# Performance work log

Measured on AMD Instinct MI355X. Metric: run time of the kernel, lower is better.

## Reference

```python
import math
import jax, jax.numpy as jnp
import numpy as np

NUM_HEADS = 16


def apply_rope(q, k, position_ids, dim):
    # q, k: [N, S, H, Dh]; position_ids: [S]
    half = dim // 2
    j = jnp.arange(half, dtype=q.dtype)
    theta = 1.0 / (10000.0 ** (2.0 * j / dim))                 # [half]
    angles = position_ids.astype(jnp.float32)[:, None] * theta[None, :]  # [S, half]
    cos = jnp.cos(angles)[None, :, None, :]                    # [1, S, 1, half]
    sin = jnp.sin(angles)[None, :, None, :]
    q1, q2 = q[..., :half], q[..., half:]
    k1, k2 = k[..., :half], k[..., half:]
    q_rot = jnp.concatenate([q1 * cos - q2 * sin, q1 * sin + q2 * cos], axis=-1)
    k_rot = jnp.concatenate([k1 * cos - k2 * sin, k1 * sin + k2 * cos], axis=-1)
    return q_rot, k_rot


def setup_inputs() -> dict:
    key = jax.random.key(0)
    ks = jax.random.split(key, 6)
    N, S, H = 2, 2048, 2048
    scale = 1.0 / math.sqrt(H)  # ~xavier magnitude
    X = jax.random.normal(ks[0], (N, S, H), dtype=jnp.float32)
    Wq = jax.random.normal(ks[1], (H, H), dtype=jnp.float32) * scale
    Wk = jax.random.normal(ks[2], (H, H), dtype=jnp.float32) * scale
    Wv = jax.random.normal(ks[3], (H, H), dtype=jnp.float32) * scale
    Wo = jax.random.normal(ks[4], (H, H), dtype=jnp.float32) * scale
    bo = jnp.zeros((H,), dtype=jnp.float32)
    position_ids = jnp.arange(S, dtype=jnp.int64 if jax.config.jax_enable_x64 else jnp.int32)
    mask = jnp.tril(jnp.ones((S, S), dtype=jnp.int32))  # causal
    return {"X": X, "position_ids": position_ids, "mask": mask,
            "Wq": Wq, "Wk": Wk, "Wv": Wv, "Wo": Wo, "bo": bo}


def reference(X, position_ids, mask, Wq, Wk, Wv, Wo, bo):
    N, S, H = X.shape
    nh = NUM_HEADS
    dh = H // nh
    # projections -> [N, S, nh, dh]
    Q = (X @ Wq.T).reshape(N, S, nh, dh)
    K = (X @ Wk.T).reshape(N, S, nh, dh)
    V = (X @ Wv.T).reshape(N, S, nh, dh)
    Q, K = apply_rope(Q, K, position_ids, dh)
    scores = jnp.einsum('bqhd,bkhd->bhqk', Q, K) / math.sqrt(dh)  # [N, nh, S, S]
    scores = jnp.where(mask[None, None, :, :] == 0, -jnp.inf, scores)
    weights = jax.nn.softmax(scores, axis=-1)
    context = jnp.einsum('bhqk,bkhd->bqhd', weights, V).reshape(N, S, H)
    return context @ Wo.T + bo
```

## Files before the change

### kernel.cpp

```cpp
#include <hip/hip_runtime.h>
#include <hip/hip_bf16.h>
#include <stdint.h>

typedef unsigned short u16;
typedef __attribute__((ext_vector_type(4))) float f32x4;
typedef __attribute__((ext_vector_type(8))) short s16x8;
typedef __attribute__((ext_vector_type(8))) __bf16 b16x8;

constexpr int NB = 2, SEQ = 2048, HD = 2048, NHEADS = 16, DHEAD = 128;
constexpr int MROWS = NB * SEQ;

__device__ __forceinline__ u16 f2b(float f) {
  __hip_bfloat16 h = __float2bfloat16(f);
  return __builtin_bit_cast(u16, h);
}
__device__ __forceinline__ float b2f(u16 u) {
  return __bfloat162float(__builtin_bit_cast(__hip_bfloat16, u));
}
__device__ __forceinline__ f32x4 mfma_bf16(s16x8 a, s16x8 b, f32x4 c) {
  return __builtin_amdgcn_mfma_f32_16x16x32_bf16(
      __builtin_bit_cast(b16x8, a), __builtin_bit_cast(b16x8, b), c, 0, 0, 0);
}
__device__ __forceinline__ void gload_lds16(const void* g, void* l) {
  __builtin_amdgcn_global_load_lds(
      (__attribute__((address_space(1))) void*)(const_cast<void*>(g)),
      (__attribute__((address_space(3))) void*)(l), 16, 0, 0);
}

__global__ void cvt_bf16(const float* __restrict__ in, u16* __restrict__ out, int n8) {
  int i = blockIdx.x * blockDim.x + threadIdx.x;
  if (i >= n8) return;
  const float4* p = (const float4*)(in + (size_t)i * 8);
  float4 a = p[0], b = p[1];
  ushort4* q = (ushort4*)(out + (size_t)i * 8);
  q[0] = make_ushort4(f2b(a.x), f2b(a.y), f2b(a.z), f2b(a.w));
  q[1] = make_ushort4(f2b(b.x), f2b(b.y), f2b(b.z), f2b(b.w));
}

template <bool FBIAS>
__global__ __launch_bounds__(256, 2) void gemm_nt(
    const u16* __restrict__ A, const u16* __restrict__ B, void* __restrict__ Cv,
    const float* __restrict__ bias, int Kd, int Nd) {
  __shared__ __align__(16) u16 Alds[128 * 32];
  __shared__ __align__(16) u16 Blds[128 * 32];
  const int t = threadIdx.x;
  const int lane = t & 63, w = t >> 6;
  const int lr = lane & 15, lg = lane >> 4;
  const int wr = (w >> 1) * 64, wc = (w & 1) * 64;
  const int trow = blockIdx.y * 128, tcol = blockIdx.x * 128;

  f32x4 acc[4][4] = {};

  const int c0 = t, c1 = t + 256;
  const u16* gA0 = A + (size_t)(trow + (c0 >> 2)) * Kd + (c0 & 3) * 8;
  const u16* gA1 = A + (size_t)(trow + (c1 >> 2)) * Kd + (c1 & 3) * 8;
  const u16* gB0 = B + (size_t)(tcol + (c0 >> 2)) * Kd + (c0 & 3) * 8;
  const u16* gB1 = B + (size_t)(tcol + (c1 >> 2)) * Kd + (c1 & 3) * 8;
  u16* lA0 = Alds + c0 * 8; u16* lA1 = Alds + c1 * 8;
  u16* lB0 = Blds + c0 * 8; u16* lB1 = Blds + c1 * 8;

  for (int kk = 0; kk < Kd; kk += 32) {
    gload_lds16(gA0 + kk, lA0);
    gload_lds16(gA1 + kk, lA1);
    gload_lds16(gB0 + kk, lB0);
    gload_lds16(gB1 + kk, lB1);
    __syncthreads();
    s16x8 af[4], bf[4];
#pragma unroll
    for (int m = 0; m < 4; ++m)
      af[m] = *(const s16x8*)(Alds + (wr + m * 16 + lr) * 32 + lg * 8);
#pragma unroll
    for (int nn = 0; nn < 4; ++nn)
      bf[nn] = *(const s16x8*)(Blds + (wc + nn * 16 + lr) * 32 + lg * 8);
#pragma unroll
    for (int m = 0; m < 4; ++m)
#pragma unroll
      for (int nn = 0; nn < 4; ++nn)
        acc[m][nn] = mfma_bf16(af[m], bf[nn], acc[m][nn]);
    __syncthreads();
  }

#pragma unroll
  for (int m = 0; m < 4; ++m)
#pragma unroll
    for (int nn = 0; nn < 4; ++nn)
#pragma unroll
      for (int r = 0; r < 4; ++r) {
        int row = trow + wr + m * 16 + lg * 4 + r;
        int col = tcol + wc + nn * 16 + lr;
        if constexpr (FBIAS)
          ((float*)Cv)[(size_t)row * Nd + col] = acc[m][nn][r] + bias[col];
        else
          ((u16*)Cv)[(size_t)row * Nd + col] = f2b(acc[m][nn][r]);
      }
}

__global__ void rope_inplace(u16* __restrict__ Qb, u16* __restrict__ Kb,
                             const int* __restrict__ pos) {
  int idx = blockIdx.x * blockDim.x + threadIdx.x;
  int row = idx >> 10;
  int pr = idx & 1023;
  int h = pr >> 6, j = pr & 63;
  int s = row & (SEQ - 1);
  float theta = expf(-0.14391156831f * (float)j);
  float ang = (float)pos[s] * theta;
  float sn, cs;
  sincosf(ang, &sn, &cs);
  size_t base = (size_t)row * HD + h * 128 + j;
  float q1 = b2f(Qb[base]), q2 = b2f(Qb[base + 64]);
  Qb[base] = f2b(q1 * cs - q2 * sn);
  Qb[base + 64] = f2b(q1 * sn + q2 * cs);
  float k1 = b2f(Kb[base]), k2 = b2f(Kb[base + 64]);
  Kb[base] = f2b(k1 * cs - k2 * sn);
  Kb[base + 64] = f2b(k1 * sn + k2 * cs);
}

__global__ __launch_bounds__(256, 4) void attn_fwd(
    const u16* __restrict__ Qb, const u16* __restrict__ Kb,
    const u16* __restrict__ Vt, u16* __restrict__ Ctx) {
  __shared__ __align__(16) u16 Klds[64 * 128];
  __shared__ __align__(16) u16 Vlds[128 * 64];
  __shared__ __align__(16) u16 Plds[4][16 * 64];

  const int t = threadIdx.x;
  const int lane = t & 63, w = t >> 6;
  const int lr = lane & 15, lg = lane >> 4;
  const int qt = (int)gridDim.x - 1 - (int)blockIdx.x;
  const int h = blockIdx.y, n = blockIdx.z;
  const int q0 = qt * 64 + w * 16;
  const size_t hoff = (size_t)h * DHEAD;

  s16x8 qf[4];
#pragma unroll
  for (int c = 0; c < 4; ++c)
    qf[c] = *(const s16x8*)(Qb + (size_t)(n * SEQ + q0 + lr) * HD + hoff + c * 32 + lg * 8);

  f32x4 o[8] = {};
  float mrow[4] = {-1e30f, -1e30f, -1e30f, -1e30f};
  float lsum[4] = {0.f, 0.f, 0.f, 0.f};

  const int nkt = qt + 1;

  for (int kt = 0; kt < nkt; ++kt) {
#pragma unroll
    for (int p = 0; p < 4; ++p) {
      int q = p * 256 + t;
      int r = q >> 4, cs = (q & 15) ^ (r & 7);
      gload_lds16(Kb + (size_t)(n * SEQ + kt * 64 + r) * HD + hoff + cs * 8,
                  Klds + q * 8);
    }
#pragma unroll
    for (int p = 0; p < 4; ++p) {
      int q = p * 256 + t;
      int r = q >> 3, cs = (q & 7) ^ (r & 7);
      gload_lds16(Vt + (size_t)(hoff + r) * MROWS + n * SEQ + kt * 64 + cs * 8,
                  Vlds + q * 8);
    }
    __syncthreads();

    f32x4 sc[4];
#pragma unroll
    for (int kb = 0; kb < 4; ++kb) {
      f32x4 a = {0.f, 0.f, 0.f, 0.f};
#pragma unroll
      for (int c = 0; c < 4; ++c) {
        s16x8 kf = *(const s16x8*)(Klds + (kb * 16 + lr) * 128 +
                                   (((c * 4 + lg) ^ (lr & 7))) * 8);
        a = mfma_bf16(qf[c], kf, a);
      }
      sc[kb] = a;
    }

    constexpr float scale = 0.08838834764831845f;
    float tmax[4] = {-1e30f, -1e30f, -1e30f, -1e30f};
#pragma unroll
    for (int r = 0; r < 4; ++r) {
      int qg = q0 + lg * 4 + r;
#pragma unroll
      for (int kb = 0; kb < 4; ++kb) {
        float s = sc[kb][r] * scale;
        if (kt * 64 + kb * 16 + lr > qg) s = -1e30f;
        sc[kb][r] = s;
        tmax[r] = fmaxf(tmax[r], s);
      }
    }
#pragma unroll
    for (int off = 1; off < 16; off <<= 1)
#pragma unroll
      for (int r = 0; r < 4; ++r)
        tmax[r] = fmaxf(tmax[r], __shfl_xor(tmax[r], off));

    float corr[4], rsum[4];
#pragma unroll
    for (int r = 0; r < 4; ++r) {
      float mnew = fmaxf(mrow[r], tmax[r]);
      corr[r] = __expf(mrow[r] - mnew);
      mrow[r] = mnew;
      rsum[r] = 0.f;
      int prow = lg * 4 + r;
#pragma unroll
      for (int kb = 0; kb < 4; ++kb) {
        float pv = __expf(sc[kb][r] - mnew);
        rsum[r] += pv;
        int col = kb * 16 + lr;
        Plds[w][prow * 64 + ((col >> 3) ^ (prow & 7)) * 8 + (col & 7)] = f2b(pv);
      }
    }
#pragma unroll
    for (int off = 1; off < 16; off <<= 1)
#pragma unroll
      for (int r = 0; r < 4; ++r) rsum[r] += __shfl_xor(rsum[r], off);
#pragma unroll
    for (int r = 0; r < 4; ++r) lsum[r] = lsum[r] * corr[r] + rsum[r];
#pragma unroll
    for (int nb = 0; nb < 8; ++nb)
#pragma unroll
      for (int r = 0; r < 4; ++r) o[nb][r] *= corr[r];

    s16x8 pf0 = *(const s16x8*)(&Plds[w][lr * 64 + ((lg) ^ (lr & 7)) * 8]);
    s16x8 pf1 = *(const s16x8*)(&Plds[w][lr * 64 + ((4 + lg) ^ (lr & 7)) * 8]);
#pragma unroll
    for (int nb = 0; nb < 8; ++nb) {
      int vrow = nb * 16 + lr;
      s16x8 vf0 = *(const s16x8*)(Vlds + vrow * 64 + ((lg) ^ (lr & 7)) * 8);
      s16x8 vf1 = *(const s16x8*)(Vlds + vrow * 64 + ((4 + lg) ^ (lr & 7)) * 8);
      o[nb] = mfma_bf16(pf0, vf0, o[nb]);
      o[nb] = mfma_bf16(pf1, vf1, o[nb]);
    }
    __syncthreads();
  }

  float inv[4];
#pragma unroll
  for (int r = 0; r < 4; ++r) inv[r] = 1.0f / lsum[r];
#pragma unroll
  for (int nb = 0; nb < 8; ++nb)
#pragma unroll
    for (int r = 0; r < 4; ++r)
      Ctx[(size_t)(n * SEQ + q0 + lg * 4 + r) * HD + hoff + nb * 16 + lr] =
          f2b(o[nb][r] * inv[r]);
}

extern "C" void kernel_launch(void* const* d_in, const int* in_sizes, int n_in,
                              void* d_out, int out_size, void* d_ws, size_t ws_size,
                              hipStream_t stream) {
  (void)in_sizes; (void)n_in; (void)out_size; (void)ws_size;
  const float* X  = (const float*)d_in[0];
  const int*  pos = (const int*)d_in[1];
  const float* Wq = (const float*)d_in[3];
  const float* Wk = (const float*)d_in[4];
  const float* Wv = (const float*)d_in[5];
  const float* Wo = (const float*)d_in[6];
  const float* bo = (const float*)d_in[7];
  float* out = (float*)d_out;

  constexpr size_t XE = (size_t)MROWS * HD;
  constexpr size_t WE = (size_t)HD * HD;

  char* p = (char*)d_ws;
  u16* Xb  = (u16*)p; p += XE * 2;
  u16* Wqb = (u16*)p; p += WE * 2;
  u16* Wkb = (u16*)p; p += WE * 2;
  u16* Wvb = (u16*)p; p += WE * 2;
  u16* Wob = (u16*)p; p += WE * 2;
  u16* Qb  = (u16*)p; p += XE * 2;
  u16* Kb  = (u16*)p; p += XE * 2;
  u16* Vtb = (u16*)p; p += XE * 2;
  u16* Ctx = Xb;

  cvt_bf16<<<(int)(XE / 8 / 256), 256, 0, stream>>>(X, Xb, (int)(XE / 8));
  cvt_bf16<<<(int)(WE / 8 / 256), 256, 0, stream>>>(Wq, Wqb, (int)(WE / 8));
  cvt_bf16<<<(int)(WE / 8 / 256), 256, 0, stream>>>(Wk, Wkb, (int)(WE / 8));
  cvt_bf16<<<(int)(WE / 8 / 256), 256, 0, stream>>>(Wv, Wvb, (int)(WE / 8));
  cvt_bf16<<<(int)(WE / 8 / 256), 256, 0, stream>>>(Wo, Wob, (int)(WE / 8));

  dim3 g(HD / 128, MROWS / 128);
  gemm_nt<false><<<g, 256, 0, stream>>>(Xb, Wqb, Qb, nullptr, HD, HD);
  gemm_nt<false><<<g, 256, 0, stream>>>(Xb, Wkb, Kb, nullptr, HD, HD);
  dim3 gv(MROWS / 128, HD / 128);
  gemm_nt<false><<<gv, 256, 0, stream>>>(Wvb, Xb, Vtb, nullptr, HD, MROWS);

  rope_inplace<<<MROWS * 1024 / 256, 256, 0, stream>>>(Qb, Kb, pos);

  attn_fwd<<<dim3(SEQ / 64, NHEADS, NB), 256, 0, stream>>>(Qb, Kb, Vtb, Ctx);

  gemm_nt<true><<<g, 256, 0, stream>>>(Ctx, Wob, out, bo, HD, HD);
}
```

Before: 547.7 us.

## Rewrite attention kernel with double-buffered K/V, transposed MFMA, and lazy rescaling

Reworks the flash-attention kernel. It now uses 512-thread blocks with 128 query rows each, double-buffers K/V tiles in LDS so the next tile loads while the current one computes, and swaps the MFMA operands so each lane owns one query row. That removes the cross-lane shuffles for row max and sum. The softmax scale and log2(e) are folded into Q during RoPE so exp2f can be used. Rescaling is skipped unless the running max grows by more than a threshold, fully masked tiles per wave are skipped, and blocks are remapped for XCD locality. LDS use and register pressure go up, and the lazy rescale threshold carries some numerical risk.

```diff
diff --git a/kernel.cpp b/kernel.cpp
--- a/kernel.cpp
+++ b/kernel.cpp
@@ -97,6 +97,7 @@
 
 __global__ void rope_inplace(u16* __restrict__ Qb, u16* __restrict__ Kb,
                              const int* __restrict__ pos) {
+  const float QSC = 0.08838834764831845f * 1.4426950408889634f;
   int idx = blockIdx.x * blockDim.x + threadIdx.x;
   int row = idx >> 10;
   int pr = idx & 1023;
@@ -108,137 +109,156 @@
   sincosf(ang, &sn, &cs);
   size_t base = (size_t)row * HD + h * 128 + j;
   float q1 = b2f(Qb[base]), q2 = b2f(Qb[base + 64]);
-  Qb[base] = f2b(q1 * cs - q2 * sn);
-  Qb[base + 64] = f2b(q1 * sn + q2 * cs);
+  Qb[base] = f2b((q1 * cs - q2 * sn) * QSC);
+  Qb[base + 64] = f2b((q1 * sn + q2 * cs) * QSC);
   float k1 = b2f(Kb[base]), k2 = b2f(Kb[base + 64]);
   Kb[base] = f2b(k1 * cs - k2 * sn);
   Kb[base + 64] = f2b(k1 * sn + k2 * cs);
 }
 
-__global__ __launch_bounds__(256, 4) void attn_fwd(
+__global__ __launch_bounds__(512, 4) void attn_fwd(
     const u16* __restrict__ Qb, const u16* __restrict__ Kb,
     const u16* __restrict__ Vt, u16* __restrict__ Ctx) {
-  __shared__ __align__(16) u16 Klds[64 * 128];
-  __shared__ __align__(16) u16 Vlds[128 * 64];
-  __shared__ __align__(16) u16 Plds[4][16 * 64];
+  constexpr int KSZ = 64 * 128;
+  __shared__ __align__(16) u16 Klds[2 * KSZ];
+  __shared__ __align__(16) u16 Vlds[2 * KSZ];
+  __shared__ __align__(16) u16 Plds[8 * 1024];
 
   const int t = threadIdx.x;
   const int lane = t & 63, w = t >> 6;
   const int lr = lane & 15, lg = lane >> 4;
-  const int qt = (int)gridDim.x - 1 - (int)blockIdx.x;
-  const int h = blockIdx.y, n = blockIdx.z;
-  const int q0 = qt * 64 + w * 16;
+
+  const int f = blockIdx.x;
+  const int xcd = f & 7, j = f >> 3;
+  const int pp = xcd + 8 * (j >> 4);
+  const int qt = 15 - (j & 15);
+  const int h = pp & 15, n = pp >> 4;
+
+  const int q0 = qt * 128 + w * 16;
+  const int qg = q0 + lr;
   const size_t hoff = (size_t)h * DHEAD;
 
+  const int kq0 = t, kq1 = t + 512;
+  const int kr0 = kq0 >> 4, kr1 = kq1 >> 4;
+  const u16* gK0 = Kb + (size_t)(n * SEQ + kr0) * HD + hoff + ((kq0 & 15) ^ (kr0 & 7)) * 8;
+  const u16* gK1 = Kb + (size_t)(n * SEQ + kr1) * HD + hoff + ((kq1 & 15) ^ (kr1 & 7)) * 8;
+  u16* lK0 = Klds + kq0 * 8;
+  u16* lK1 = Klds + kq1 * 8;
+  const int vr0 = kq0 >> 3, vr1 = kq1 >> 3;
+  const u16* gV0 = Vt + (size_t)(hoff + vr0) * MROWS + n * SEQ + ((kq0 & 7) ^ (vr0 & 7)) * 8;
+  const u16* gV1 = Vt + (size_t)(hoff + vr1) * MROWS + n * SEQ + ((kq1 & 7) ^ (vr1 & 7)) * 8;
+  u16* lV0 = Vlds + kq0 * 8;
+  u16* lV1 = Vlds + kq1 * 8;
+
   s16x8 qf[4];
 #pragma unroll
   for (int c = 0; c < 4; ++c)
-    qf[c] = *(const s16x8*)(Qb + (size_t)(n * SEQ + q0 + lr) * HD + hoff + c * 32 + lg * 8);
+    qf[c] = *(const s16x8*)(Qb + (size_t)(n * SEQ + qg) * HD + hoff + c * 32 + lg * 8);
 
   f32x4 o[8] = {};
-  float mrow[4] = {-1e30f, -1e30f, -1e30f, -1e30f};
-  float lsum[4] = {0.f, 0.f, 0.f, 0.f};
-
-  const int nkt = qt + 1;
+  float mrow = -3.0e38f, lsum = 0.f;
+  u16* PW = Plds + w * 1024;
+
+  const int nkt = 2 * qt + 2;
+
+  gload_lds16(gK0, lK0);
+  gload_lds16(gK1, lK1);
+  gload_lds16(gV0, lV0);
+  gload_lds16(gV1, lV1);
+  __syncthreads();
 
   for (int kt = 0; kt < nkt; ++kt) {
-#pragma unroll
-    for (int p = 0; p < 4; ++p) {
-      int q = p * 256 + t;
-      int r = q >> 4, cs = (q & 15) ^ (r & 7);
-      gload_lds16(Kb + (size_t)(n * SEQ + kt * 64 + r) * HD + hoff + cs * 8,
-                  Klds + q * 8);
+    const int cur = kt & 1;
+    const u16* Kc = Klds + cur * KSZ;
+    const u16* Vc = Vlds + cur * KSZ;
+    const int ktb = kt * 64;
+
+    if (kt + 1 < nkt) {
+      const int b1 = (cur ^ 1) * KSZ;
+      const size_t ko = (size_t)(kt + 1) * 64 * HD;
+      const int vo = (kt + 1) * 64;
+      gload_lds16(gK0 + ko, lK0 + b1);
+      gload_lds16(gK1 + ko, lK1 + b1);
+      gload_lds16(gV0 + vo, lV0 + b1);
+      gload_lds16(gV1 + vo, lV1 + b1);
     }
-#pragma unroll
-    for (int p = 0; p < 4; ++p) {
-      int q = p * 256 + t;
-      int r = q >> 3, cs = (q & 7) ^ (r & 7);
-      gload_lds16(Vt + (size_t)(hoff + r) * MROWS + n * SEQ + kt * 64 + cs * 8,
-                  Vlds + q * 8);
-    }
-    __syncthreads();
-
-    f32x4 sc[4];
-#pragma unroll
-    for (int kb = 0; kb < 4; ++kb) {
-      f32x4 a = {0.f, 0.f, 0.f, 0.f};
-#pragma unroll
-      for (int c = 0; c < 4; ++c) {
-        s16x8 kf = *(const s16x8*)(Klds + (kb * 16 + lr) * 128 +
-                                   (((c * 4 + lg) ^ (lr & 7))) * 8);
-        a = mfma_bf16(qf[c], kf, a);
-      }
-      sc[kb] = a;
-    }
-
-    constexpr float scale = 0.08838834764831845f;
-    float tmax[4] = {-1e30f, -1e30f, -1e30f, -1e30f};
-#pragma unroll
-    for (int r = 0; r < 4; ++r) {
-      int qg = q0 + lg * 4 + r;
+
+    if (ktb <= q0 + 15) {
+      f32x4 sc[4];
 #pragma unroll
       for (int kb = 0; kb < 4; ++kb) {
-        float s = sc[kb][r] * scale;
-        if (kt * 64 + kb * 16 + lr > qg) s = -1e30f;
-        sc[kb][r] = s;
-        tmax[r] = fmaxf(tmax[r], s);
-      }
-    }
-#pragma unroll
-    for (int off = 1; off < 16; off <<= 1)
-#pragma unroll
-      for (int r = 0; r < 4; ++r)
-        tmax[r] = fmaxf(tmax[r], __shfl_xor(tmax[r], off));
-
-    float corr[4], rsum[4];
-#pragma unroll
-    for (int r = 0; r < 4; ++r) {
-      float mnew = fmaxf(mrow[r], tmax[r]);
-      corr[r] = __expf(mrow[r] - mnew);
-      mrow[r] = mnew;
-      rsum[r] = 0.f;
-      int prow = lg * 4 + r;
+        f32x4 a = {0.f, 0.f, 0.f, 0.f};
+        const u16* krow = Kc + (kb * 16 + lr) * 128;
+#pragma unroll
+        for (int c = 0; c < 4; ++c) {
+          s16x8 kf = *(const s16x8*)(krow + ((c * 4 + lg) ^ (lr & 7)) * 8);
+          a = mfma_bf16(kf, qf[c], a);
+        }
+        sc[kb] = a;
+      }
+
+      if (ktb + 63 > q0) {
+#pragma unroll
+        for (int kb = 0; kb < 4; ++kb)
+#pragma unroll
+          for (int r = 0; r < 4; ++r)
+            if (ktb + kb * 16 + lg * 4 + r > qg) sc[kb][r] = -3.0e38f;
+      }
+
+      float tm = -3.0e38f;
+#pragma unroll
+      for (int kb = 0; kb < 4; ++kb)
+#pragma unroll
+        for (int r = 0; r < 4; ++r) tm = fmaxf(tm, sc[kb][r]);
+      tm = fmaxf(tm, __shfl_xor(tm, 16));
+      tm = fmaxf(tm, __shfl_xor(tm, 32));
+      if (!__all(tm - mrow <= 8.0f)) {
+        float mn = fmaxf(mrow, tm);
+        float corr = exp2f(mrow - mn);
+        mrow = mn;
+        lsum *= corr;
+#pragma unroll
+        for (int nb = 0; nb < 8; ++nb)
+#pragma unroll
+          for (int r = 0; r < 4; ++r) o[nb][r] *= corr;
+      }
+
+      float rs = 0.f;
 #pragma unroll
       for (int kb = 0; kb < 4; ++kb) {
-        float pv = __expf(sc[kb][r] - mnew);
-        rsum[r] += pv;
-        int col = kb * 16 + lr;
-        Plds[w][prow * 64 + ((col >> 3) ^ (prow & 7)) * 8 + (col & 7)] = f2b(pv);
-      }
-    }
-#pragma unroll
-    for (int off = 1; off < 16; off <<= 1)
-#pragma unroll
-      for (int r = 0; r < 4; ++r) rsum[r] += __shfl_xor(rsum[r], off);
-#pragma unroll
-    for (int r = 0; r < 4; ++r) lsum[r] = lsum[r] * corr[r] + rsum[r];
-#pragma unroll
-    for (int nb = 0; nb < 8; ++nb)
-#pragma unroll
-      for (int r = 0; r < 4; ++r) o[nb][r] *= corr[r];
-
-    s16x8 pf0 = *(const s16x8*)(&Plds[w][lr * 64 + ((lg) ^ (lr & 7)) * 8]);
-    s16x8 pf1 = *(const s16x8*)(&Plds[w][lr * 64 + ((4 + lg) ^ (lr & 7)) * 8]);
-#pragma unroll
-    for (int nb = 0; nb < 8; ++nb) {
-      int vrow = nb * 16 + lr;
-      s16x8 vf0 = *(const s16x8*)(Vlds + vrow * 64 + ((lg) ^ (lr & 7)) * 8);
-      s16x8 vf1 = *(const s16x8*)(Vlds + vrow * 64 + ((4 + lg) ^ (lr & 7)) * 8);
-      o[nb] = mfma_bf16(pf0, vf0, o[nb]);
-      o[nb] = mfma_bf16(pf1, vf1, o[nb]);
+        float p0 = exp2f(sc[kb][0] - mrow);
+        float p1 = exp2f(sc[kb][1] - mrow);
+        float p2 = exp2f(sc[kb][2] - mrow);
+        float p3 = exp2f(sc[kb][3] - mrow);
+        rs += (p0 + p1) + (p2 + p3);
+        *(ushort4*)(PW + lr * 64 + ((kb * 16 + lg * 4) ^ ((lr & 7) * 8))) =
+            make_ushort4(f2b(p0), f2b(p1), f2b(p2), f2b(p3));
+      }
+      rs += __shfl_xor(rs, 16);
+      rs += __shfl_xor(rs, 32);
+      lsum += rs;
+
+      s16x8 pf0 = *(const s16x8*)(PW + lr * 64 + ((lg ^ (lr & 7))) * 8);
+      s16x8 pf1 = *(const s16x8*)(PW + lr * 64 + (((4 + lg) ^ (lr & 7))) * 8);
+#pragma unroll
+      for (int nb = 0; nb < 8; ++nb) {
+        const u16* vrow = Vc + (nb * 16 + lr) * 64;
+        s16x8 vf0 = *(const s16x8*)(vrow + ((lg ^ (lr & 7))) * 8);
+        s16x8 vf1 = *(const s16x8*)(vrow + (((4 + lg) ^ (lr & 7))) * 8);
+        o[nb] = mfma_bf16(vf0, pf0, o[nb]);
+        o[nb] = mfma_bf16(vf1, pf1, o[nb]);
+      }
     }
     __syncthreads();
   }
 
-  float inv[4];
-#pragma unroll
-  for (int r = 0; r < 4; ++r) inv[r] = 1.0f / lsum[r];
+  const float inv = 1.0f / lsum;
+  u16* crow = Ctx + (size_t)(n * SEQ + qg) * HD + hoff;
 #pragma unroll
   for (int nb = 0; nb < 8; ++nb)
-#pragma unroll
-    for (int r = 0; r < 4; ++r)
-      Ctx[(size_t)(n * SEQ + q0 + lg * 4 + r) * HD + hoff + nb * 16 + lr] =
-          f2b(o[nb][r] * inv[r]);
+    *(ushort4*)(crow + nb * 16 + lg * 4) =
+        make_ushort4(f2b(o[nb][0] * inv), f2b(o[nb][1] * inv),
+                     f2b(o[nb][2] * inv), f2b(o[nb][3] * inv));
 }
 
 extern "C" void kernel_launch(void* const* d_in, const int* in_sizes, int n_in,
@@ -282,7 +302,7 @@
 
   rope_inplace<<<MROWS * 1024 / 256, 256, 0, stream>>>(Qb, Kb, pos);
 
-  attn_fwd<<<dim3(SEQ / 64, NHEADS, NB), 256, 0, stream>>>(Qb, Kb, Vtb, Ctx);
+  attn_fwd<<<dim3(512), 512, 0, stream>>>(Qb, Kb, Vtb, Ctx);
 
   gemm_nt<true><<<g, 256, 0, stream>>>(Ctx, Wob, out, bo, HD, HD);
 }
```

Measured after the change: 462.1 us. -15.6%, faster.
